# Kernel tuning notes

Measured on AMD Instinct MI355X. Metric: run time of the kernel, lower is better.

Reference implementation:

```python
import jax, jax.numpy as jnp
import numpy as np

B, H, S, E = 16384, 16, 1, 64
N_OTHERS = 4


def setup_inputs() -> dict:
    key = jax.random.key(0)
    ks = jax.random.split(key, N_OTHERS + 2)
    inp = {f"others_{i}": jax.random.normal(ks[i], (B, H, S, E), dtype=jnp.float32)
           for i in range(N_OTHERS)}
    inp["main"] = jax.random.normal(ks[N_OTHERS], (B, H, S, E), dtype=jnp.float32)
    inp["W"] = jax.random.normal(ks[N_OTHERS + 1], (E, E), dtype=jnp.float32) * (1.0 / np.sqrt(E))
    return inp


def reference(others_0, others_1, others_2, others_3, main, W):
    # mean over the 'others' modalities: (B, H, 1, E)
    mean = (others_0 + others_1 + others_2 + others_3) / 4.0
    m = jnp.squeeze(mean, 2)        # (B, H, E)
    main_sq = jnp.squeeze(main, 2)  # (B, H, E)
    # bilinear score: mean @ W @ main^T -> (B, H, H)
    score = jnp.einsum('bhe,ef,bgf->bhg', m, W, main_sq)
    attn = jax.nn.softmax(score, axis=-1)      # (B, H, H)
    context = jnp.einsum('bhg,bge->bhe', attn, main_sq)  # (B, H, E)
    return context, attn
```

## Files before the change

### kernel.cpp

```cpp
#include <hip/hip_runtime.h>

#define NBATCH 16384
#define H 16
#define E 64
#define NB 4
#define NWAVE 4
#define NBLK (NBATCH / (NB * NWAVE))

typedef __attribute__((ext_vector_type(8))) short short8v;
typedef __attribute__((ext_vector_type(4))) float f32x4;

#define CFENCE asm volatile("" ::: "memory")

__device__ __forceinline__ unsigned short f2bf(float x) {
    return (unsigned short)(__float_as_uint(x) >> 16);
}
__device__ __forceinline__ float bfres(float x) {
    return x - __uint_as_float(__float_as_uint(x) & 0xFFFF0000u);
}

#define BSPLIT8(HIv, LOv, A, B) do { \
    HIv[0]=(short)f2bf(A.x); LOv[0]=(short)f2bf(bfres(A.x)); \
    HIv[1]=(short)f2bf(A.y); LOv[1]=(short)f2bf(bfres(A.y)); \
    HIv[2]=(short)f2bf(A.z); LOv[2]=(short)f2bf(bfres(A.z)); \
    HIv[3]=(short)f2bf(A.w); LOv[3]=(short)f2bf(bfres(A.w)); \
    HIv[4]=(short)f2bf(B.x); LOv[4]=(short)f2bf(bfres(B.x)); \
    HIv[5]=(short)f2bf(B.y); LOv[5]=(short)f2bf(bfres(B.y)); \
    HIv[6]=(short)f2bf(B.z); LOv[6]=(short)f2bf(bfres(B.z)); \
    HIv[7]=(short)f2bf(B.w); LOv[7]=(short)f2bf(bfres(B.w)); \
} while (0)

#define FMA4(ACC, S, B) do { \
    ACC.x = fmaf(S, B.x, ACC.x); ACC.y = fmaf(S, B.y, ACC.y); \
    ACC.z = fmaf(S, B.z, ACC.z); ACC.w = fmaf(S, B.w, ACC.w); } while (0)

#define SMAX1(X, OUT) do { \
    float mx_ = (X); \
    mx_ = fmaxf(mx_, __shfl_xor(mx_, 1)); \
    mx_ = fmaxf(mx_, __shfl_xor(mx_, 2)); \
    mx_ = fmaxf(mx_, __shfl_xor(mx_, 4)); \
    mx_ = fmaxf(mx_, __shfl_xor(mx_, 8)); \
    float e_ = __expf((X) - mx_); \
    float sm_ = e_; \
    sm_ += __shfl_xor(sm_, 1); \
    sm_ += __shfl_xor(sm_, 2); \
    sm_ += __shfl_xor(sm_, 4); \
    sm_ += __shfl_xor(sm_, 8); \
    OUT = e_ * __builtin_amdgcn_rcpf(sm_); \
} while (0)

__global__ __launch_bounds__(256, 1) void ovo_kernel(
    const float* __restrict__ o0, const float* __restrict__ o1,
    const float* __restrict__ o2, const float* __restrict__ o3,
    const float* __restrict__ mn, const float* __restrict__ W,
    float* __restrict__ ctx_out, float* __restrict__ attn_out)
{
    __shared__ __align__(16) unsigned short sWfrag[4][2][2][512];
    __shared__ float sT[NWAVE][2][H * 68];

    const int tid = threadIdx.x;
    const int l   = tid & 63;
    const int wv  = tid >> 6;
    const int r   = l & 15;
    const int q   = l >> 4;

    float4 po0[4], po1[4], po2[4], po3[4];
    {
        const size_t base = (size_t)(blockIdx.x * NWAVE + wv) * (H * E);
#pragma unroll
        for (int sc = 0; sc < 4; ++sc) {
            const int s = sc >> 1, c01 = sc & 1;
            const size_t off = base + r * 64 + 32 * s + 8 * q + 4 * c01;
            po0[sc] = *(const float4*)(o0 + off);
            po1[sc] = *(const float4*)(o1 + off);
            po2[sc] = *(const float4*)(o2 + off);
            po3[sc] = *(const float4*)(o3 + off);
        }
    }

    for (int rr = 0; rr < 16; ++rr) {
        const int flat = rr * 256 + tid;
        const float w = W[flat];
        const int e = flat >> 6, f = flat & 63;
        const int t = f >> 4, col = f & 15;
        const int s = e >> 5, khi = (e >> 3) & 3, i = e & 7;
        const int L = col + 16 * khi;
        sWfrag[t][s][0][L * 8 + i] = f2bf(w);
        sWfrag[t][s][1][L * 8 + i] = f2bf(bfres(w));
    }
    __syncthreads();

    float* const sU    = &sT[wv][0][0];
    float* const sMain = &sT[wv][1][0];

#pragma unroll 1
    for (int it = 0; it < NB; ++it) {
        const int batch = it * (NBLK * NWAVE) + blockIdx.x * NWAVE + wv;
        const size_t base = (size_t)batch * (H * E);

        short8v ahi[2], alo[2];
#pragma unroll
        for (int s = 0; s < 2; ++s) {
            const int sa = s * 2, sb = s * 2 + 1;
            float4 mA, mB;
            mA.x = ((po0[sa].x + po1[sa].x) + (po2[sa].x + po3[sa].x)) * 0.25f;
            mA.y = ((po0[sa].y + po1[sa].y) + (po2[sa].y + po3[sa].y)) * 0.25f;
            mA.z = ((po0[sa].z + po1[sa].z) + (po2[sa].z + po3[sa].z)) * 0.25f;
            mA.w = ((po0[sa].w + po1[sa].w) + (po2[sa].w + po3[sa].w)) * 0.25f;
            mB.x = ((po0[sb].x + po1[sb].x) + (po2[sb].x + po3[sb].x)) * 0.25f;
            mB.y = ((po0[sb].y + po1[sb].y) + (po2[sb].y + po3[sb].y)) * 0.25f;
            mB.z = ((po0[sb].z + po1[sb].z) + (po2[sb].z + po3[sb].z)) * 0.25f;
            mB.w = ((po0[sb].w + po1[sb].w) + (po2[sb].w + po3[sb].w)) * 0.25f;
            BSPLIT8(ahi[s], alo[s], mA, mB);
        }

        float4 pm0 = *(const float4*)(mn + base + 0 * 256 + l * 4);
        float4 pm1 = *(const float4*)(mn + base + 1 * 256 + l * 4);
        float4 pm2 = *(const float4*)(mn + base + 2 * 256 + l * 4);
        float4 pm3 = *(const float4*)(mn + base + 3 * 256 + l * 4);

        if (it + 1 < NB) {
            const size_t nbase = base + (size_t)(NBLK * NWAVE) * (H * E);
#pragma unroll
            for (int sc = 0; sc < 4; ++sc) {
                const int s = sc >> 1, c01 = sc & 1;
                const size_t off = nbase + r * 64 + 32 * s + 8 * q + 4 * c01;
                po0[sc] = *(const float4*)(o0 + off);
                po1[sc] = *(const float4*)(o1 + off);
                po2[sc] = *(const float4*)(o2 + off);
                po3[sc] = *(const float4*)(o3 + off);
            }
        }
        CFENCE;

#pragma unroll
        for (int t = 0; t < 4; ++t) {
            short8v bh0 = *(const short8v*)&sWfrag[t][0][0][l * 8];
            short8v bl0 = *(const short8v*)&sWfrag[t][0][1][l * 8];
            short8v bh1 = *(const short8v*)&sWfrag[t][1][0][l * 8];
            short8v bl1 = *(const short8v*)&sWfrag[t][1][1][l * 8];
            f32x4 acc = {0.f, 0.f, 0.f, 0.f};
            acc = __builtin_amdgcn_mfma_f32_16x16x32_bf16(ahi[0], bh0, acc, 0, 0, 0);
            acc = __builtin_amdgcn_mfma_f32_16x16x32_bf16(alo[0], bh0, acc, 0, 0, 0);
            acc = __builtin_amdgcn_mfma_f32_16x16x32_bf16(ahi[0], bl0, acc, 0, 0, 0);
            acc = __builtin_amdgcn_mfma_f32_16x16x32_bf16(ahi[1], bh1, acc, 0, 0, 0);
            acc = __builtin_amdgcn_mfma_f32_16x16x32_bf16(alo[1], bh1, acc, 0, 0, 0);
            acc = __builtin_amdgcn_mfma_f32_16x16x32_bf16(ahi[1], bl1, acc, 0, 0, 0);
#pragma unroll
            for (int j = 0; j < 4; ++j)
                sU[(4 * q + j) * 68 + 16 * t + r] = acc[j];
        }
        CFENCE;

        {
            const int f0 = l * 4;
            *(float4*)&sMain[((f0) >> 6) * 68 + (f0 & 63)] = pm0;
            *(float4*)&sMain[((f0 + 256) >> 6) * 68 + (f0 & 63)] = pm1;
            *(float4*)&sMain[((f0 + 512) >> 6) * 68 + (f0 & 63)] = pm2;
            *(float4*)&sMain[((f0 + 768) >> 6) * 68 + (f0 & 63)] = pm3;
        }
        CFENCE;

        f32x4 d3 = {0.f, 0.f, 0.f, 0.f};
#pragma unroll
        for (int ks = 0; ks < 2; ++ks) {
            float4 a01 = *(const float4*)&sU[r * 68 + ks * 32 + 8 * q];
            float4 a23 = *(const float4*)&sU[r * 68 + ks * 32 + 8 * q + 4];
            float4 b01 = *(const float4*)&sMain[r * 68 + ks * 32 + 8 * q];
            float4 b23 = *(const float4*)&sMain[r * 68 + ks * 32 + 8 * q + 4];
            short8v ah, al2, bh, bl2;
            BSPLIT8(ah, al2, a01, a23);
            BSPLIT8(bh, bl2, b01, b23);
            d3 = __builtin_amdgcn_mfma_f32_16x16x32_bf16(ah,  bh,  d3, 0, 0, 0);
            d3 = __builtin_amdgcn_mfma_f32_16x16x32_bf16(al2, bh,  d3, 0, 0, 0);
            d3 = __builtin_amdgcn_mfma_f32_16x16x32_bf16(ah,  bl2, d3, 0, 0, 0);
        }
        CFENCE;

        float4 at4;
        SMAX1(d3[0], at4.x);
        SMAX1(d3[1], at4.y);
        SMAX1(d3[2], at4.z);
        SMAX1(d3[3], at4.w);
        *(float4*)&sU[r * 20 + 4 * q] = at4;
        {
            float* ap = attn_out + (size_t)batch * (H * H);
            ap[(4 * q + 0) * 16 + r] = at4.x;
            ap[(4 * q + 1) * 16 + r] = at4.y;
            ap[(4 * q + 2) * 16 + r] = at4.z;
            ap[(4 * q + 3) * 16 + r] = at4.w;
        }
        CFENCE;

        {
            const int h0 = q * 4, e0c = r * 4;
            float4 c0 = {0.f,0.f,0.f,0.f}, c1 = {0.f,0.f,0.f,0.f};
            float4 c2 = {0.f,0.f,0.f,0.f}, c3 = {0.f,0.f,0.f,0.f};
#pragma unroll
            for (int g = 0; g < 16; ++g) {
                float4 bvv = *(const float4*)&sMain[g * 68 + e0c];
                float4 avv = *(const float4*)&sU[g * 20 + h0];
                FMA4(c0, avv.x, bvv);
                FMA4(c1, avv.y, bvv);
                FMA4(c2, avv.z, bvv);
                FMA4(c3, avv.w, bvv);
            }
            float* cp = ctx_out + base;
            *(float4*)(cp + (h0 + 0) * 64 + e0c) = c0;
            *(float4*)(cp + (h0 + 1) * 64 + e0c) = c1;
            *(float4*)(cp + (h0 + 2) * 64 + e0c) = c2;
            *(float4*)(cp + (h0 + 3) * 64 + e0c) = c3;
        }
        CFENCE;
    }
}

extern "C" void kernel_launch(void* const* d_in, const int* in_sizes, int n_in,
                              void* d_out, int out_size, void* d_ws, size_t ws_size,
                              hipStream_t stream) {
    const float* o0 = (const float*)d_in[0];
    const float* o1 = (const float*)d_in[1];
    const float* o2 = (const float*)d_in[2];
    const float* o3 = (const float*)d_in[3];
    const float* mn = (const float*)d_in[4];
    const float* W  = (const float*)d_in[5];
    float* ctx  = (float*)d_out;
    float* attn = ctx + (size_t)NBATCH * H * E;
    hipLaunchKernelGGL(ovo_kernel, dim3(NBLK), dim3(NWAVE * 64), 0, stream,
                       o0, o1, o2, o3, mn, W, ctx, attn);
}
```

Measured before the change: 86.78 us.

## Use grid-stride persistent loop and prefetch main rows in MFMA fragment layout

Replaces the fixed 1024-block, 4-iteration schedule with a 768-block grid-stride loop over batch groups, which changes the work split across CUs (some blocks now run 5 groups, others 6). The main tensor is now loaded in the same per-lane layout as the MFMA B operand. Those registers feed the score MFMAs directly instead of being read back from shared memory, and the next group's main rows are prefetched one iteration ahead, alongside the others prefetch. The initial loads are moved after the W fragment setup. The cost is more live registers and uneven per-block trip counts.

```diff
diff --git a/kernel.cpp b/kernel.cpp
--- a/kernel.cpp
+++ b/kernel.cpp
@@ -3,9 +3,9 @@
 #define NBATCH 16384
 #define H 16
 #define E 64
-#define NB 4
 #define NWAVE 4
-#define NBLK (NBATCH / (NB * NWAVE))
+#define NGRID 768
+#define NGROUP (NBATCH / NWAVE)
 
 typedef __attribute__((ext_vector_type(8))) short short8v;
 typedef __attribute__((ext_vector_type(4))) float f32x4;
@@ -63,20 +63,7 @@
     const int wv  = tid >> 6;
     const int r   = l & 15;
     const int q   = l >> 4;
-
-    float4 po0[4], po1[4], po2[4], po3[4];
-    {
-        const size_t base = (size_t)(blockIdx.x * NWAVE + wv) * (H * E);
-#pragma unroll
-        for (int sc = 0; sc < 4; ++sc) {
-            const int s = sc >> 1, c01 = sc & 1;
-            const size_t off = base + r * 64 + 32 * s + 8 * q + 4 * c01;
-            po0[sc] = *(const float4*)(o0 + off);
-            po1[sc] = *(const float4*)(o1 + off);
-            po2[sc] = *(const float4*)(o2 + off);
-            po3[sc] = *(const float4*)(o3 + off);
-        }
-    }
+    const int bid = blockIdx.x;
 
     for (int rr = 0; rr < 16; ++rr) {
         const int flat = rr * 256 + tid;
@@ -88,15 +75,36 @@
         sWfrag[t][s][0][L * 8 + i] = f2bf(w);
         sWfrag[t][s][1][L * 8 + i] = f2bf(bfres(w));
     }
+
+    float4 po0[4], po1[4], po2[4], po3[4];
+    float4 pmA, pmB, pmC, pmD;
+    {
+        const size_t base = (size_t)(bid * NWAVE + wv) * (H * E);
+#pragma unroll
+        for (int sc = 0; sc < 4; ++sc) {
+            const int s = sc >> 1, c01 = sc & 1;
+            const size_t off = base + r * 64 + 32 * s + 8 * q + 4 * c01;
+            po0[sc] = *(const float4*)(o0 + off);
+            po1[sc] = *(const float4*)(o1 + off);
+            po2[sc] = *(const float4*)(o2 + off);
+            po3[sc] = *(const float4*)(o3 + off);
+        }
+        pmA = *(const float4*)(mn + base + r * 64 +      8 * q);
+        pmB = *(const float4*)(mn + base + r * 64 +      8 * q + 4);
+        pmC = *(const float4*)(mn + base + r * 64 + 32 + 8 * q);
+        pmD = *(const float4*)(mn + base + r * 64 + 32 + 8 * q + 4);
+    }
     __syncthreads();
 
     float* const sU    = &sT[wv][0][0];
     float* const sMain = &sT[wv][1][0];
 
 #pragma unroll 1
-    for (int it = 0; it < NB; ++it) {
-        const int batch = it * (NBLK * NWAVE) + blockIdx.x * NWAVE + wv;
+    for (int g = bid; g < NGROUP; g += NGRID) {
+        const int batch = g * NWAVE + wv;
         const size_t base = (size_t)batch * (H * E);
+        const size_t nbase = (size_t)((g + NGRID) * NWAVE + wv) * (H * E);
+        const bool more = (g + NGRID) < NGROUP;
 
         short8v ahi[2], alo[2];
 #pragma unroll
@@ -114,13 +122,7 @@
             BSPLIT8(ahi[s], alo[s], mA, mB);
         }
 
-        float4 pm0 = *(const float4*)(mn + base + 0 * 256 + l * 4);
-        float4 pm1 = *(const float4*)(mn + base + 1 * 256 + l * 4);
-        float4 pm2 = *(const float4*)(mn + base + 2 * 256 + l * 4);
-        float4 pm3 = *(const float4*)(mn + base + 3 * 256 + l * 4);
-
-        if (it + 1 < NB) {
-            const size_t nbase = base + (size_t)(NBLK * NWAVE) * (H * E);
+        if (more) {
 #pragma unroll
             for (int sc = 0; sc < 4; ++sc) {
                 const int s = sc >> 1, c01 = sc & 1;
@@ -150,30 +152,41 @@
             for (int j = 0; j < 4; ++j)
                 sU[(4 * q + j) * 68 + 16 * t + r] = acc[j];
         }
-        CFENCE;
-
-        {
-            const int f0 = l * 4;
-            *(float4*)&sMain[((f0) >> 6) * 68 + (f0 & 63)] = pm0;
-            *(float4*)&sMain[((f0 + 256) >> 6) * 68 + (f0 & 63)] = pm1;
-            *(float4*)&sMain[((f0 + 512) >> 6) * 68 + (f0 & 63)] = pm2;
-            *(float4*)&sMain[((f0 + 768) >> 6) * 68 + (f0 & 63)] = pm3;
-        }
+
+        *(float4*)&sMain[r * 68 +      8 * q]     = pmA;
+        *(float4*)&sMain[r * 68 +      8 * q + 4] = pmB;
+        *(float4*)&sMain[r * 68 + 32 + 8 * q]     = pmC;
+        *(float4*)&sMain[r * 68 + 32 + 8 * q + 4] = pmD;
         CFENCE;
 
         f32x4 d3 = {0.f, 0.f, 0.f, 0.f};
-#pragma unroll
-        for (int ks = 0; ks < 2; ++ks) {
-            float4 a01 = *(const float4*)&sU[r * 68 + ks * 32 + 8 * q];
-            float4 a23 = *(const float4*)&sU[r * 68 + ks * 32 + 8 * q + 4];
-            float4 b01 = *(const float4*)&sMain[r * 68 + ks * 32 + 8 * q];
-            float4 b23 = *(const float4*)&sMain[r * 68 + ks * 32 + 8 * q + 4];
+        {
+            float4 a01 = *(const float4*)&sU[r * 68 + 8 * q];
+            float4 a23 = *(const float4*)&sU[r * 68 + 8 * q + 4];
             short8v ah, al2, bh, bl2;
             BSPLIT8(ah, al2, a01, a23);
-            BSPLIT8(bh, bl2, b01, b23);
+            BSPLIT8(bh, bl2, pmA, pmB);
             d3 = __builtin_amdgcn_mfma_f32_16x16x32_bf16(ah,  bh,  d3, 0, 0, 0);
             d3 = __builtin_amdgcn_mfma_f32_16x16x32_bf16(al2, bh,  d3, 0, 0, 0);
             d3 = __builtin_amdgcn_mfma_f32_16x16x32_bf16(ah,  bl2, d3, 0, 0, 0);
+        }
+        {
+            float4 a01 = *(const float4*)&sU[r * 68 + 32 + 8 * q];
+            float4 a23 = *(const float4*)&sU[r * 68 + 32 + 8 * q + 4];
+            short8v ah, al2, bh, bl2;
+            BSPLIT8(ah, al2, a01, a23);
+            BSPLIT8(bh, bl2, pmC, pmD);
+            d3 = __builtin_amdgcn_mfma_f32_16x16x32_bf16(ah,  bh,  d3, 0, 0, 0);
+            d3 = __builtin_amdgcn_mfma_f32_16x16x32_bf16(al2, bh,  d3, 0, 0, 0);
+            d3 = __builtin_amdgcn_mfma_f32_16x16x32_bf16(ah,  bl2, d3, 0, 0, 0);
+        }
+        CFENCE;
+
+        if (more) {
+            pmA = *(const float4*)(mn + nbase + r * 64 +      8 * q);
+            pmB = *(const float4*)(mn + nbase + r * 64 +      8 * q + 4);
+            pmC = *(const float4*)(mn + nbase + r * 64 + 32 + 8 * q);
+            pmD = *(const float4*)(mn + nbase + r * 64 + 32 + 8 * q + 4);
         }
         CFENCE;
 
@@ -197,9 +210,9 @@
             float4 c0 = {0.f,0.f,0.f,0.f}, c1 = {0.f,0.f,0.f,0.f};
             float4 c2 = {0.f,0.f,0.f,0.f}, c3 = {0.f,0.f,0.f,0.f};
 #pragma unroll
-            for (int g = 0; g < 16; ++g) {
-                float4 bvv = *(const float4*)&sMain[g * 68 + e0c];
-                float4 avv = *(const float4*)&sU[g * 20 + h0];
+            for (int gg = 0; gg < 16; ++gg) {
+                float4 bvv = *(const float4*)&sMain[gg * 68 + e0c];
+                float4 avv = *(const float4*)&sU[gg * 20 + h0];
                 FMA4(c0, avv.x, bvv);
                 FMA4(c1, avv.y, bvv);
                 FMA4(c2, avv.z, bvv);
@@ -226,6 +239,6 @@
     const float* W  = (const float*)d_in[5];
     float* ctx  = (float*)d_out;
     float* attn = ctx + (size_t)NBATCH * H * E;
-    hipLaunchKernelGGL(ovo_kernel, dim3(NBLK), dim3(NWAVE * 64), 0, stream,
+    hipLaunchKernelGGL(ovo_kernel, dim3(NGRID), dim3(NWAVE * 64), 0, stream,
                        o0, o1, o2, o3, mn, W, ctx, attn);
 }
```

After: 84.60 us. -2.5%, faster.
